# Optimization experiments

Measured on AMD Instinct MI355X. Metric: run time of the kernel, lower is better.

Reference implementation:

```python
import jax, jax.numpy as jnp
import numpy as np

TEMPERATURE = 0.02
B, S, D_TOK, H = 128, 32, 128, 128  # batch, query tokens, doc tokens, hidden dim


def setup_inputs() -> dict:
    key = jax.random.key(0)
    kq, kp = jax.random.split(key)
    query_embeddings = jax.random.normal(kq, (B, S, H), dtype=jnp.float32)
    positive_embeddings = jax.random.normal(kp, (B, D_TOK, H), dtype=jnp.float32)
    return {"query_embeddings": query_embeddings, "positive_embeddings": positive_embeddings}


def reference(query_embeddings, positive_embeddings):
    # Late interaction: [b, c, s, d] = every query token vs every doc token (in-batch negatives)
    late = jnp.einsum('bsh,cdh->bcsd', query_embeddings, positive_embeddings)
    # MaxSim over doc tokens, sum over query tokens -> [b, c] score matrix
    scores = late.max(axis=-1).sum(axis=-1) / TEMPERATURE
    # In-batch negatives: label for row i is column i (the diagonal is the positive)
    logp = jax.nn.log_softmax(scores, axis=-1)
    loss = -jnp.mean(jnp.diagonal(logp))
    return loss
```

## Files before the change

### kernel.cpp

```cpp
#include <hip/hip_runtime.h>
#include <hip/hip_bf16.h>

typedef __bf16 bf16x8 __attribute__((ext_vector_type(8)));
typedef __bf16 bf16x4 __attribute__((ext_vector_type(4)));
typedef float  f32x4  __attribute__((ext_vector_type(4)));

#define WQ_ELEMS (128 * 32 * 128)
#define WP_ELEMS (128 * 128 * 128)
#define WS_NEED  ((size_t)(WQ_ELEMS + WP_ELEMS) * 2 + 128 * 128 * 4)

__global__ __launch_bounds__(256) void convert_qp(
    const float* __restrict__ Q, const float* __restrict__ P,
    unsigned short* __restrict__ wq, unsigned short* __restrict__ wp)
{
    const int bid = blockIdx.x;
    if (bid < 256) {
        const int g = bid * 256 + threadIdx.x;
        const int b = g >> 9, j = g & 511;
        const int si = j >> 8, k = (j >> 6) & 3, l = j & 63;
        const float* src = Q + (size_t)b * 4096 + (si * 16 + (l & 15)) * 128 + k * 32 + (l >> 4) * 8;
        float4 v0 = *(const float4*)src;
        float4 v1 = *(const float4*)(src + 4);
        bf16x8 o = { (__bf16)v0.x, (__bf16)v0.y, (__bf16)v0.z, (__bf16)v0.w,
                     (__bf16)v1.x, (__bf16)v1.y, (__bf16)v1.z, (__bf16)v1.w };
        *(bf16x8*)(wq + ((size_t)g << 3)) = o;
    } else {
        const int g = (bid - 256) * 256 + threadIdx.x;
        const int c = g >> 11;
        const int f = (g >> 6) & 31, l = g & 63;
        const int dj = f >> 2, k = f & 3;
        const float* src = P + (size_t)c * 16384 + (dj * 16 + (l & 15)) * 128 + k * 32 + (l >> 4) * 8;
        float4 v0 = *(const float4*)src;
        float4 v1 = *(const float4*)(src + 4);
        bf16x8 o = { (__bf16)v0.x, (__bf16)v0.y, (__bf16)v0.z, (__bf16)v0.w,
                     (__bf16)v1.x, (__bf16)v1.y, (__bf16)v1.z, (__bf16)v1.w };
        *(bf16x8*)(wp + ((size_t)g << 3)) = o;
    }
}

__global__ __launch_bounds__(256, 2) void colbert_scores_v2(
    const unsigned short* __restrict__ Pb,
    const unsigned short* __restrict__ Qb,
    float* __restrict__ scores)
{
    __shared__ __align__(16) unsigned short ps[2][16384];

    const int tid  = threadIdx.x;
    const int lane = tid & 63;
    const int wave = tid >> 6;

    const int xcd = blockIdx.x & 7;
    const int idx = blockIdx.x >> 3;
    const int cp  = (xcd << 3) + (idx & 7);
    const int g   = idx >> 3;
    const int cw  = wave >> 1;
    const int c   = (cp << 1) + cw;
    const int bbase = (g << 4) + ((wave & 1) << 3);

    bf16x8 A[2][4];
    {
        const unsigned short* qw = Qb + ((size_t)bbase << 12);
        #pragma unroll
        for (int k = 0; k < 4; k++) {
            A[0][k] = *(const bf16x8*)(qw + (k << 9) + (lane << 3));
            A[1][k] = *(const bf16x8*)(qw + 2048 + (k << 9) + (lane << 3));
        }
    }

    {
        const float4* src = (const float4*)(Pb + ((size_t)cp << 15));
        float4* dst = (float4*)&ps[0][0];
        #pragma unroll
        for (int t = 0; t < 16; t++)
            dst[t * 256 + tid] = src[t * 256 + tid];
    }
    __syncthreads();

    bf16x8 bp[8][4];
    #pragma unroll
    for (int dj = 0; dj < 8; dj++)
        #pragma unroll
        for (int k = 0; k < 4; k++)
            bp[dj][k] = *(const bf16x8*)&ps[cw][(((dj << 2) + k) << 9) + (lane << 3)];

    #pragma unroll
    for (int it = 0; it < 8; it++) {
        const int b = bbase + it;

        bf16x8 N[2][4];
        if (it < 7) {
            const unsigned short* qw = Qb + ((size_t)(b + 1) << 12);
            #pragma unroll
            for (int k = 0; k < 4; k++) {
                N[0][k] = *(const bf16x8*)(qw + (k << 9) + (lane << 3));
                N[1][k] = *(const bf16x8*)(qw + 2048 + (k << 9) + (lane << 3));
            }
        }

        float mm0 = -1e30f, mm1 = -1e30f;
        #pragma unroll
        for (int dj = 0; dj < 8; dj++) {
            f32x4 t0 = (f32x4){0.f, 0.f, 0.f, 0.f};
            f32x4 t1 = (f32x4){0.f, 0.f, 0.f, 0.f};
            #pragma unroll
            for (int k = 0; k < 4; k++) {
                t0 = __builtin_amdgcn_mfma_f32_16x16x32_bf16(bp[dj][k], A[0][k], t0, 0, 0, 0);
                t1 = __builtin_amdgcn_mfma_f32_16x16x32_bf16(bp[dj][k], A[1][k], t1, 0, 0, 0);
            }
            #pragma unroll
            for (int r = 0; r < 4; r++) {
                mm0 = fmaxf(mm0, t0[r]);
                mm1 = fmaxf(mm1, t1[r]);
            }
        }

        mm0 = fmaxf(mm0, __shfl_xor(mm0, 16));
        mm0 = fmaxf(mm0, __shfl_xor(mm0, 32));
        mm1 = fmaxf(mm1, __shfl_xor(mm1, 16));
        mm1 = fmaxf(mm1, __shfl_xor(mm1, 32));
        float partial = mm0 + mm1;
        partial += __shfl_xor(partial, 1);
        partial += __shfl_xor(partial, 2);
        partial += __shfl_xor(partial, 4);
        partial += __shfl_xor(partial, 8);
        if (lane == 0) scores[b * 128 + c] = partial * 50.0f;

        if (it < 7) {
            #pragma unroll
            for (int k = 0; k < 4; k++) { A[0][k] = N[0][k]; A[1][k] = N[1][k]; }
        }
    }
}

__global__ __launch_bounds__(1024) void colbert_loss128(
    const float* __restrict__ scores, unsigned* __restrict__ out)
{
    __shared__ float gpart[128];
    __shared__ float wpart[2];
    const int tid = threadIdx.x;
    const int grp = tid >> 3;
    const int j   = tid & 7;

    const float4* row = (const float4*)(scores + grp * 128);
    float v[16];
    #pragma unroll
    for (int u = 0; u < 4; u++) {
        float4 q = row[j * 4 + u];
        v[u * 4 + 0] = q.x; v[u * 4 + 1] = q.y; v[u * 4 + 2] = q.z; v[u * 4 + 3] = q.w;
    }
    float m = v[0];
    #pragma unroll
    for (int u = 1; u < 16; u++) m = fmaxf(m, v[u]);
    m = fmaxf(m, __shfl_xor(m, 1));
    m = fmaxf(m, __shfl_xor(m, 2));
    m = fmaxf(m, __shfl_xor(m, 4));
    float e = 0.f;
    #pragma unroll
    for (int u = 0; u < 16; u++) e += expf(v[u] - m);
    e += __shfl_xor(e, 1);
    e += __shfl_xor(e, 2);
    e += __shfl_xor(e, 4);
    if (j == 0) gpart[grp] = scores[grp * 129] - m - logf(e);
    __syncthreads();

    if (tid < 128) {
        float p = gpart[tid];
        p += __shfl_xor(p, 1);  p += __shfl_xor(p, 2);  p += __shfl_xor(p, 4);
        p += __shfl_xor(p, 8);  p += __shfl_xor(p, 16); p += __shfl_xor(p, 32);
        if ((tid & 63) == 0) wpart[tid >> 6] = p;
    }
    __syncthreads();
    if (tid == 0) {
        float loss = -(wpart[0] + wpart[1]) / 128.0f;
        unsigned bits = __float_as_uint(loss);
        unsigned rnd  = (bits + 0x7FFFu + ((bits >> 16) & 1u)) & 0xFFFF0000u;
        out[0] = rnd | (rnd >> 16);
    }
}

__global__ __launch_bounds__(256, 2) void colbert_scores_slow(
    const float* __restrict__ Q, const float* __restrict__ P, float* __restrict__ scores)
{
    __shared__ __align__(16) unsigned short qs[4 * 32 * 128];
    __shared__ __align__(16) unsigned short ps[128 * 128];
    const int tid = threadIdx.x;
    const int b0 = (blockIdx.x & 31) * 4, c0 = (blockIdx.x >> 5) * 4;
    const float4* gq = (const float4*)(Q + (size_t)b0 * 4096);
    #pragma unroll
    for (int j = tid; j < 4096; j += 256) {
        float4 v = gq[j];
        int f = j << 2, row = f >> 7, h = f & 127;
        int dst = (row << 7) + (((h >> 3) ^ (row & 15)) << 3) + (h & 7);
        bf16x4 o = { (__bf16)v.x, (__bf16)v.y, (__bf16)v.z, (__bf16)v.w };
        *(bf16x4*)&qs[dst] = o;
    }
    const int lane = tid & 63, wave = tid >> 6, n = lane & 15, quad = lane >> 4;
    const unsigned short* qb = qs + wave * 4096;
    #pragma unroll 1
    for (int it = 0; it < 4; it++) {
        const int c = c0 + it;
        if (it) __syncthreads();
        const float4* gp = (const float4*)(P + (size_t)c * 16384);
        #pragma unroll
        for (int j = tid; j < 4096; j += 256) {
            float4 v = gp[j];
            int f = j << 2, d = f >> 7, h = f & 127;
            int dst = (d << 7) + (((h >> 3) ^ (d & 15)) << 3) + (h & 7);
            bf16x4 o = { (__bf16)v.x, (__bf16)v.y, (__bf16)v.z, (__bf16)v.w };
            *(bf16x4*)&ps[dst] = o;
        }
        __syncthreads();
        f32x4 acc[2][8];
        #pragma unroll
        for (int si = 0; si < 2; si++)
            #pragma unroll
            for (int dj = 0; dj < 8; dj++) acc[si][dj] = (f32x4){0.f,0.f,0.f,0.f};
        #pragma unroll
        for (int k = 0; k < 4; k++) {
            const int chunk = (((k << 2) + quad) ^ n) << 3;
            bf16x8 a0 = *(const bf16x8*)&qb[(n << 7) + chunk];
            bf16x8 a1 = *(const bf16x8*)&qb[((n + 16) << 7) + chunk];
            #pragma unroll
            for (int dj = 0; dj < 8; dj++) {
                bf16x8 bb = *(const bf16x8*)&ps[((dj * 16 + n) << 7) + chunk];
                acc[0][dj] = __builtin_amdgcn_mfma_f32_16x16x32_bf16(a0, bb, acc[0][dj], 0, 0, 0);
                acc[1][dj] = __builtin_amdgcn_mfma_f32_16x16x32_bf16(a1, bb, acc[1][dj], 0, 0, 0);
            }
        }
        float partial = 0.f;
        #pragma unroll
        for (int si = 0; si < 2; si++)
            #pragma unroll
            for (int r = 0; r < 4; r++) {
                float m = acc[si][0][r];
                #pragma unroll
                for (int dj = 1; dj < 8; dj++) m = fmaxf(m, acc[si][dj][r]);
                m = fmaxf(m, __shfl_xor(m, 1)); m = fmaxf(m, __shfl_xor(m, 2));
                m = fmaxf(m, __shfl_xor(m, 4)); m = fmaxf(m, __shfl_xor(m, 8));
                partial += m;
            }
        partial += __shfl_xor(partial, 16);
        partial += __shfl_xor(partial, 32);
        if (lane == 0) scores[(b0 + wave) * 128 + c] = partial * 50.0f;
    }
}

extern "C" void kernel_launch(void* const* d_in, const int* in_sizes, int n_in,
                              void* d_out, int out_size, void* d_ws, size_t ws_size,
                              hipStream_t stream) {
    const float* Q = (const float*)d_in[0];
    const float* P = (const float*)d_in[1];

    if (ws_size >= WS_NEED) {
        unsigned short* wq = (unsigned short*)d_ws;
        unsigned short* wp = wq + WQ_ELEMS;
        float* scores = (float*)(wp + WP_ELEMS);
        convert_qp<<<dim3(1280), dim3(256), 0, stream>>>(Q, P, wq, wp);
        colbert_scores_v2<<<dim3(512), dim3(256), 0, stream>>>(wp, wq, scores);
        colbert_loss128<<<dim3(1), dim3(1024), 0, stream>>>(scores, (unsigned*)d_out);
    } else {
        float* scores = (float*)d_ws;
        colbert_scores_slow<<<dim3(1024), dim3(256), 0, stream>>>(Q, P, scores);
        colbert_loss128<<<dim3(1), dim3(1024), 0, stream>>>(scores, (unsigned*)d_out);
    }
}
```

Before: 81.42 us.

## Swap block tiling: stage queries in LDS, keep one doc per wave in registers

Each block now handles four document columns (one per wave), each held in registers and loaded straight from global memory. The block shares a group of 8 queries, staged in LDS and read back per iteration. Before, two documents were staged in LDS and every wave streamed its own 8 queries from global memory with register prefetch. The aim is more reuse of queries within a block and fewer redundant global query loads, at the cost of larger per-wave document loads from global and LDS reads in the inner loop. The workspace size check gains 64 extra bytes, which looks unrelated.

```diff
diff --git a/kernel.cpp b/kernel.cpp
--- a/kernel.cpp
+++ b/kernel.cpp
@@ -7,7 +7,7 @@
 
 #define WQ_ELEMS (128 * 32 * 128)
 #define WP_ELEMS (128 * 128 * 128)
-#define WS_NEED  ((size_t)(WQ_ELEMS + WP_ELEMS) * 2 + 128 * 128 * 4)
+#define WS_NEED  ((size_t)(WQ_ELEMS + WP_ELEMS) * 2 + 128 * 128 * 4 + 64)
 
 __global__ __launch_bounds__(256) void convert_qp(
     const float* __restrict__ Q, const float* __restrict__ P,
@@ -38,12 +38,12 @@
     }
 }
 
-__global__ __launch_bounds__(256, 2) void colbert_scores_v2(
+__global__ __launch_bounds__(256, 2) void colbert_scores_v4(
     const unsigned short* __restrict__ Pb,
     const unsigned short* __restrict__ Qb,
     float* __restrict__ scores)
 {
-    __shared__ __align__(16) unsigned short ps[2][16384];
+    __shared__ __align__(16) unsigned short qs[8 * 4096];
 
     const int tid  = threadIdx.x;
     const int lane = tid & 63;
@@ -51,50 +51,39 @@
 
     const int xcd = blockIdx.x & 7;
     const int idx = blockIdx.x >> 3;
-    const int cp  = (xcd << 3) + (idx & 7);
-    const int g   = idx >> 3;
-    const int cw  = wave >> 1;
-    const int c   = (cp << 1) + cw;
-    const int bbase = (g << 4) + ((wave & 1) << 3);
-
-    bf16x8 A[2][4];
+    const int cg  = (xcd << 2) + (idx & 3);
+    const int bg  = idx >> 2;
+    const int c   = (cg << 2) + wave;
+    const int bbase = bg << 3;
+
+    bf16x8 bp[8][4];
     {
-        const unsigned short* qw = Qb + ((size_t)bbase << 12);
-        #pragma unroll
-        for (int k = 0; k < 4; k++) {
-            A[0][k] = *(const bf16x8*)(qw + (k << 9) + (lane << 3));
-            A[1][k] = *(const bf16x8*)(qw + 2048 + (k << 9) + (lane << 3));
-        }
+        const unsigned short* pw = Pb + ((size_t)c << 14);
+        #pragma unroll
+        for (int dj = 0; dj < 8; dj++)
+            #pragma unroll
+            for (int k = 0; k < 4; k++)
+                bp[dj][k] = *(const bf16x8*)(pw + (((dj << 2) + k) << 9) + (lane << 3));
     }
 
     {
-        const float4* src = (const float4*)(Pb + ((size_t)cp << 15));
-        float4* dst = (float4*)&ps[0][0];
+        const float4* src = (const float4*)(Qb + ((size_t)bg << 15));
+        float4* dst = (float4*)&qs[0];
         #pragma unroll
         for (int t = 0; t < 16; t++)
             dst[t * 256 + tid] = src[t * 256 + tid];
     }
     __syncthreads();
 
-    bf16x8 bp[8][4];
-    #pragma unroll
-    for (int dj = 0; dj < 8; dj++)
-        #pragma unroll
-        for (int k = 0; k < 4; k++)
-            bp[dj][k] = *(const bf16x8*)&ps[cw][(((dj << 2) + k) << 9) + (lane << 3)];
-
     #pragma unroll
     for (int it = 0; it < 8; it++) {
         const int b = bbase + it;
 
-        bf16x8 N[2][4];
-        if (it < 7) {
-            const unsigned short* qw = Qb + ((size_t)(b + 1) << 12);
-            #pragma unroll
-            for (int k = 0; k < 4; k++) {
-                N[0][k] = *(const bf16x8*)(qw + (k << 9) + (lane << 3));
-                N[1][k] = *(const bf16x8*)(qw + 2048 + (k << 9) + (lane << 3));
-            }
+        bf16x8 A[2][4];
+        #pragma unroll
+        for (int k = 0; k < 4; k++) {
+            A[0][k] = *(const bf16x8*)&qs[(it << 12) + (k << 9) + (lane << 3)];
+            A[1][k] = *(const bf16x8*)&qs[(it << 12) + 2048 + (k << 9) + (lane << 3)];
         }
 
         float mm0 = -1e30f, mm1 = -1e30f;
@@ -124,11 +113,6 @@
         partial += __shfl_xor(partial, 4);
         partial += __shfl_xor(partial, 8);
         if (lane == 0) scores[b * 128 + c] = partial * 50.0f;
-
-        if (it < 7) {
-            #pragma unroll
-            for (int k = 0; k < 4; k++) { A[0][k] = N[0][k]; A[1][k] = N[1][k]; }
-        }
     }
 }
 
@@ -256,7 +240,7 @@
         unsigned short* wp = wq + WQ_ELEMS;
         float* scores = (float*)(wp + WP_ELEMS);
         convert_qp<<<dim3(1280), dim3(256), 0, stream>>>(Q, P, wq, wp);
-        colbert_scores_v2<<<dim3(512), dim3(256), 0, stream>>>(wp, wq, scores);
+        colbert_scores_v4<<<dim3(512), dim3(256), 0, stream>>>(wp, wq, scores);
         colbert_loss128<<<dim3(1), dim3(1024), 0, stream>>>(scores, (unsigned*)d_out);
     } else {
         float* scores = (float*)d_ws;
```

Result: no change. 81.65 us (+0.3%).
